# Optimization experiments

Measured on AMD Instinct MI355X. Metric: run time of the kernel, lower is better.

## Reference

```python
import jax, jax.numpy as jnp
import numpy as np

N = 8192
D_IN = 1024
D_OUT = 1024


def setup_inputs() -> dict:
    key = jax.random.key(0)
    ks = jax.random.split(key, 7)
    s = 1.0 / np.sqrt(D_IN)
    return {
        "feat": jax.random.normal(ks[0], (N, D_IN), dtype=jnp.float32),
        "Wq": jax.random.uniform(ks[1], (D_IN, D_OUT), jnp.float32, -s, s),
        "bq": jax.random.uniform(ks[2], (D_OUT,), jnp.float32, -s, s),
        "Wk": jax.random.uniform(ks[3], (D_IN, D_OUT), jnp.float32, -s, s),
        "bk": jax.random.uniform(ks[4], (D_OUT,), jnp.float32, -s, s),
        "Wv": jax.random.uniform(ks[5], (D_IN, D_OUT), jnp.float32, -s, s),
        "bv": jax.random.uniform(ks[6], (D_OUT,), jnp.float32, -s, s),
    }


def reference(feat, Wq, bq, Wk, bk, Wv, bv):
    # eval mode: dropout(p=0.3, training=False) is identity
    q = feat @ Wq + bq          # [N, D_OUT]
    k = feat @ Wk + bk          # [N, D_OUT]
    v = feat @ Wv + bv          # [N, D_OUT]
    scale = 1.0 / jnp.sqrt(jnp.float32(D_OUT))
    scores = (q @ k.T) * scale  # [N, N]
    attn = jax.nn.softmax(scores, axis=1)
    return attn @ v             # [N, D_OUT]
```

## Files before the change

### kernel.cpp

```cpp
#include <hip/hip_runtime.h>
#include <hip/hip_bf16.h>
#include <stdint.h>

typedef __hip_bfloat16 bf16;
typedef __attribute__((ext_vector_type(8))) short short8;
typedef __attribute__((ext_vector_type(4))) float f32x4;

#define BM 128
#define BN 128

__device__ __forceinline__ unsigned short f2bf_bits(float x) {
    return __builtin_bit_cast(unsigned short, __float2bfloat16(x));
}

__device__ __forceinline__ void gload_lds16(const bf16* g, bf16* l) {
    __builtin_amdgcn_global_load_lds(
        (const __attribute__((address_space(1))) void*)(const void*)g,
        (__attribute__((address_space(3))) void*)(void*)l,
        16, 0, 0);
}

__global__ void cvt_f32_bf16_x4(const float* __restrict__ in, unsigned short* __restrict__ out, int n4) {
    int i = blockIdx.x * 256 + threadIdx.x;
    if (i < n4) {
        float4 v = reinterpret_cast<const float4*>(in)[i];
        ushort4 o;
        o.x = f2bf_bits(v.x); o.y = f2bf_bits(v.y);
        o.z = f2bf_bits(v.z); o.w = f2bf_bits(v.w);
        reinterpret_cast<ushort4*>(out)[i] = o;
    }
}

__global__ void wtrans_kernel(const float* __restrict__ W0, const float* __restrict__ W1,
                              const float* __restrict__ W2, bf16* __restrict__ Wt) {
    __shared__ float tile[32][33];
    const int z = blockIdx.z;
    const float* in = (z == 0) ? W0 : (z == 1) ? W1 : W2;
    bf16* out = Wt + (size_t)z * 1024 * 1024;
    const int bx = blockIdx.x, by = blockIdx.y, tx = threadIdx.x;
    for (int r = threadIdx.y; r < 32; r += 8)
        tile[r][tx] = in[(size_t)(by * 32 + r) * 1024 + bx * 32 + tx];
    __syncthreads();
    for (int r = threadIdx.y; r < 32; r += 8)
        out[(size_t)(bx * 32 + r) * 1024 + by * 32 + tx] = __float2bfloat16(tile[tx][r]);
}

__global__ void tpose_bf16(const bf16* __restrict__ in, bf16* __restrict__ out, int rows, int cols) {
    __shared__ bf16 tile[32][33];
    const int bx = blockIdx.x, by = blockIdx.y, tx = threadIdx.x;
    for (int r = threadIdx.y; r < 32; r += 8)
        tile[r][tx] = in[(size_t)(by * 32 + r) * cols + bx * 32 + tx];
    __syncthreads();
    for (int r = threadIdx.y; r < 32; r += 8)
        out[(size_t)(bx * 32 + r) * rows + by * 32 + tx] = tile[tx][r];
}

__global__ void scale_rows(float* __restrict__ out, const float* __restrict__ lsum) {
    int i = blockIdx.x * 256 + threadIdx.x;
    float4 v = reinterpret_cast<float4*>(out)[i];
    float inv = 1.0f / lsum[i >> 8];
    v.x *= inv; v.y *= inv; v.z *= inv; v.w *= inv;
    reinterpret_cast<float4*>(out)[i] = v;
}

template <int MODE, int KH, int SWAP>
__global__ __launch_bounds__(256, 4)
void gemm_bt(const bf16* __restrict__ A, const bf16* __restrict__ B,
             const float* __restrict__ b0, const float* __restrict__ b1,
             const float* __restrict__ b2, float* __restrict__ lsum,
             bf16* __restrict__ outb, float* __restrict__ outf,
             int M, int N, int K, int ldb, int ldout, float scale) {
    constexpr int TILE = 128 * 32;
    constexpr int SELEMS = (2 * KH * TILE < 9216) ? 9216 : 2 * KH * TILE;
    __shared__ bf16 smem[SELEMS];
    bf16* As = smem;
    bf16* Bs = smem + KH * TILE;

    const int tid  = threadIdx.x;
    const int lane = tid & 63;
    const int wave = tid >> 6;
    const int wm = wave & 1, wn = wave >> 1;
    const int l16  = lane & 15;
    const int quad = lane >> 4;
    long bm0, bn0;
    if (SWAP == 2) {
        const int lin = blockIdx.y * 8 + blockIdx.x;
        const int xcd = lin & 7;
        const int s   = lin >> 3;
        bn0 = (long)(s & 7) * BN;
        bm0 = (long)((s >> 3) * 8 + xcd) * BM;
    } else {
        bm0 = (long)(SWAP ? blockIdx.y : blockIdx.x) * BM;
        bn0 = (long)(SWAP ? blockIdx.x : blockIdx.y) * BN;
    }

    const float* bias = nullptr;
    if (MODE == 0) {
        const int z = blockIdx.z;
        B    += (size_t)z * N * K;
        outb += (size_t)z * M * ldout;
        bias  = (z == 0) ? b0 : (z == 1) ? b1 : b2;
    }

    const int lrow = lane >> 2;
    const int lcol = (lane & 3) * 8;
    const bf16* gA[2][KH];
    const bf16* gB[2][KH];
    bf16* lA[2][KH];
    bf16* lB[2][KH];
#pragma unroll
    for (int u = 0; u < 2; u++)
#pragma unroll
        for (int h = 0; h < KH; h++) {
            gA[u][h] = A + (size_t)(bm0 + wave * 32 + u * 16 + lrow) * K + h * 32 + lcol;
            gB[u][h] = B + (size_t)(bn0 + wave * 32 + u * 16 + lrow) * ldb + h * 32 + lcol;
            lA[u][h] = As + h * TILE + (wave * 32 + u * 16) * 32;
            lB[u][h] = Bs + h * TILE + (wave * 32 + u * 16) * 32;
        }

    const bf16* Ard = As + (wm * 64 + l16) * 32 + quad * 8;
    const bf16* Brd = Bs + (wn * 64 + l16) * 32 + quad * 8;

    f32x4 acc[4][4];
    const f32x4 zero = {0.f, 0.f, 0.f, 0.f};
#pragma unroll
    for (int i = 0; i < 4; i++)
#pragma unroll
        for (int j = 0; j < 4; j++) acc[i][j] = zero;

    for (int k0 = 0; k0 < K; k0 += KH * 32) {
        __syncthreads();
#pragma unroll
        for (int u = 0; u < 2; u++)
#pragma unroll
            for (int h = 0; h < KH; h++) {
                gload_lds16(gA[u][h] + k0, lA[u][h]);
                gload_lds16(gB[u][h] + k0, lB[u][h]);
            }
        __syncthreads();
#pragma unroll
        for (int h = 0; h < KH; h++) {
            short8 af[4], bfr[4];
#pragma unroll
            for (int mi = 0; mi < 4; mi++)
                af[mi] = *reinterpret_cast<const short8*>(Ard + h * TILE + mi * 16 * 32);
#pragma unroll
            for (int ni = 0; ni < 4; ni++)
                bfr[ni] = *reinterpret_cast<const short8*>(Brd + h * TILE + ni * 16 * 32);
#pragma unroll
            for (int mi = 0; mi < 4; mi++)
#pragma unroll
                for (int ni = 0; ni < 4; ni++)
                    acc[mi][ni] = __builtin_amdgcn_mfma_f32_16x16x32_bf16(af[mi], bfr[ni], acc[mi][ni], 0, 0, 0);
        }
    }

    if (MODE == 0 || MODE == 1) {
        __syncthreads();
        bf16* eb = smem + wave * 1152;
        float bcol[4];
        if (MODE == 0) {
#pragma unroll
            for (int ni = 0; ni < 4; ni++) bcol[ni] = bias[bn0 + wn * 64 + l16 + ni * 16];
        }
#pragma unroll
        for (int mi = 0; mi < 4; mi++) {
#pragma unroll
            for (int r = 0; r < 4; r++) {
                float s = 0.f;
#pragma unroll
                for (int ni = 0; ni < 4; ni++) {
                    float v = acc[mi][ni][r];
                    if (MODE == 0) v += bcol[ni];
                    else { v = __expf(v * scale); s += v; }
                    eb[(quad * 4 + r) * 72 + ni * 16 + l16] = __float2bfloat16(v);
                }
                if (MODE == 1) {
                    s += __shfl_xor(s, 1);
                    s += __shfl_xor(s, 2);
                    s += __shfl_xor(s, 4);
                    s += __shfl_xor(s, 8);
                    if (l16 == 0) atomicAdd(&lsum[bm0 + wm * 64 + mi * 16 + quad * 4 + r], s);
                }
            }
            asm volatile("s_waitcnt lgkmcnt(0)" ::: "memory");
#pragma unroll
            for (int p = 0; p < 2; p++) {
                int r2 = p * 8 + (lane >> 3);
                int c2 = (lane & 7) * 8;
                short8 val = *reinterpret_cast<const short8*>(eb + r2 * 72 + c2);
                *reinterpret_cast<short8*>(
                    outb + (size_t)(bm0 + wm * 64 + mi * 16 + r2) * ldout + bn0 + wn * 64 + c2) = val;
            }
            asm volatile("s_waitcnt lgkmcnt(0)" ::: "memory");
        }
    } else {
        const int rb2 = wm * 64 + quad * 4;
        const int cb2 = wn * 64 + l16;
#pragma unroll
        for (int mi = 0; mi < 4; mi++)
#pragma unroll
            for (int r = 0; r < 4; r++) {
                long row = bm0 + rb2 + mi * 16 + r;
                float mul = (MODE == 3) ? 1.0f / lsum[row] : 0.f;
#pragma unroll
                for (int ni = 0; ni < 4; ni++) {
                    long col = bn0 + cb2 + ni * 16;
                    if (MODE == 3) outf[row * ldout + col] = acc[mi][ni][r] * mul;
                    else           outf[row * ldout + col] += acc[mi][ni][r];
                }
            }
    }
}

extern "C" void kernel_launch(void* const* d_in, const int* in_sizes, int n_in,
                              void* d_out, int out_size, void* d_ws, size_t ws_size,
                              hipStream_t stream) {
    const float* feat = (const float*)d_in[0];
    const float* Wq   = (const float*)d_in[1];
    const float* bqv  = (const float*)d_in[2];
    const float* Wk   = (const float*)d_in[3];
    const float* bkv  = (const float*)d_in[4];
    const float* Wv   = (const float*)d_in[5];
    const float* bvv  = (const float*)d_in[6];
    float* outp = (float*)d_out;

    const int M = 8192, D = 1024;
    char* ws = (char*)d_ws;
    size_t off = 0;
    auto carve = [&](size_t bytes) -> char* {
        char* r = ws + off;
        off += (bytes + 255) & ~(size_t)255;
        return r;
    };
    bf16* featb = (bf16*)carve((size_t)M * D * 2);
    bf16* Wbt   = (bf16*)carve((size_t)3 * D * D * 2);
    bf16* qkv   = (bf16*)carve((size_t)3 * M * D * 2);
    float* lsum = (float*)carve((size_t)M * 4);
    bf16* vbt   = featb;
    size_t avail = (ws_size > off) ? ws_size - off : 0;

    int C;
    if      (avail >= (size_t)M * M * 2)    C = M;
    else if (avail >= (size_t)M * 4096 * 2) C = 4096;
    else if (avail >= (size_t)M * 2048 * 2) C = 2048;
    else                                    C = 1024;
    bf16* Pc = (bf16*)carve((size_t)M * C * 2);

    {
        int n4 = M * D / 4;
        cvt_f32_bf16_x4<<<dim3((n4 + 255) / 256), dim3(256), 0, stream>>>(feat, (unsigned short*)featb, n4);
    }
    wtrans_kernel<<<dim3(32, 32, 3), dim3(32, 8), 0, stream>>>(Wq, Wk, Wv, Wbt);
    gemm_bt<0, 2, 0><<<dim3(M / 128, D / 128, 3), dim3(256), 0, stream>>>(
        featb, Wbt, bqv, bkv, bvv, nullptr, qkv, nullptr, M, D, D, D, D, 1.0f);
    tpose_bf16<<<dim3(D / 32, M / 32), dim3(32, 8), 0, stream>>>(qkv + (size_t)2 * M * D, vbt, M, D);
    hipMemsetAsync(lsum, 0, (size_t)M * 4, stream);

    const float scale = 0.03125f;
    bf16* qb = qkv;
    bf16* kb = qkv + (size_t)M * D;
    if (C == M) {
        gemm_bt<1, 2, 0><<<dim3(M / 128, M / 128), dim3(256), 0, stream>>>(
            qb, kb, nullptr, nullptr, nullptr, lsum, Pc, nullptr, M, M, D, D, M, scale);
        gemm_bt<3, 2, 2><<<dim3(D / 128, M / 128), dim3(256), 0, stream>>>(
            Pc, vbt, nullptr, nullptr, nullptr, lsum, nullptr, outp, M, D, M, M, D, 0.f);
    } else {
        hipMemsetAsync(outp, 0, (size_t)M * D * 4, stream);
        for (int c = 0; c < M / C; c++) {
            gemm_bt<1, 2, 0><<<dim3(M / 128, C / 128), dim3(256), 0, stream>>>(
                qb, kb + (size_t)c * C * D, nullptr, nullptr, nullptr, lsum, Pc, nullptr,
                M, C, D, D, C, scale);
            gemm_bt<2, 2, 1><<<dim3(D / 128, M / 128), dim3(256), 0, stream>>>(
                Pc, vbt + (size_t)c * C, nullptr, nullptr, nullptr, nullptr, nullptr, outp,
                M, D, C, M, D, 0.f);
        }
        scale_rows<<<dim3(M * D / 4 / 256), dim3(256), 0, stream>>>(outp, lsum);
    }
}
```

Measured before the change: 449.5 us.

## Split-K the PV GEMM with atomic accumulation and fuse prep kernels

Merges the feature conversion, weight transpose and lsum zeroing into a single prep launch to cut launch overhead. The attn@V GEMM (512 blocks, K=8192) is split into two K halves along grid z, so twice as many blocks run. The halves are accumulated into a zeroed output with float atomicAdd, and normalisation moves to a separate scale_rows pass. The trade-off is an extra memset, atomic traffic on an 8192x1024 fp32 output, and an extra read/write pass over the output.

```diff
diff --git a/kernel.cpp b/kernel.cpp
--- a/kernel.cpp
+++ b/kernel.cpp
@@ -20,29 +20,36 @@
         16, 0, 0);
 }
 
-__global__ void cvt_f32_bf16_x4(const float* __restrict__ in, unsigned short* __restrict__ out, int n4) {
-    int i = blockIdx.x * 256 + threadIdx.x;
-    if (i < n4) {
-        float4 v = reinterpret_cast<const float4*>(in)[i];
+__global__ void prep_kernel(const float* __restrict__ feat, unsigned short* __restrict__ featb,
+                            const float* __restrict__ W0, const float* __restrict__ W1,
+                            const float* __restrict__ W2, bf16* __restrict__ Wt,
+                            float* __restrict__ lsum) {
+    const int b = blockIdx.x;
+    const int tid = threadIdx.x;
+    if (b < 8192) {
+        int i = b * 256 + tid;
+        float4 v = reinterpret_cast<const float4*>(feat)[i];
         ushort4 o;
         o.x = f2bf_bits(v.x); o.y = f2bf_bits(v.y);
         o.z = f2bf_bits(v.z); o.w = f2bf_bits(v.w);
-        reinterpret_cast<ushort4*>(out)[i] = o;
-    }
-}
-
-__global__ void wtrans_kernel(const float* __restrict__ W0, const float* __restrict__ W1,
-                              const float* __restrict__ W2, bf16* __restrict__ Wt) {
-    __shared__ float tile[32][33];
-    const int z = blockIdx.z;
-    const float* in = (z == 0) ? W0 : (z == 1) ? W1 : W2;
-    bf16* out = Wt + (size_t)z * 1024 * 1024;
-    const int bx = blockIdx.x, by = blockIdx.y, tx = threadIdx.x;
-    for (int r = threadIdx.y; r < 32; r += 8)
-        tile[r][tx] = in[(size_t)(by * 32 + r) * 1024 + bx * 32 + tx];
-    __syncthreads();
-    for (int r = threadIdx.y; r < 32; r += 8)
-        out[(size_t)(bx * 32 + r) * 1024 + by * 32 + tx] = __float2bfloat16(tile[tx][r]);
+        reinterpret_cast<ushort4*>(featb)[i] = o;
+    } else if (b < 11264) {
+        __shared__ float tile[32][33];
+        const int b2 = b - 8192;
+        const int z = b2 >> 10;
+        const int t = b2 & 1023;
+        const int bx = t & 31, by = t >> 5;
+        const int tx = tid & 31, ty = tid >> 5;
+        const float* in = (z == 0) ? W0 : (z == 1) ? W1 : W2;
+        bf16* out = Wt + (size_t)z * 1024 * 1024;
+        for (int r = ty; r < 32; r += 8)
+            tile[r][tx] = in[(size_t)(by * 32 + r) * 1024 + bx * 32 + tx];
+        __syncthreads();
+        for (int r = ty; r < 32; r += 8)
+            out[(size_t)(bx * 32 + r) * 1024 + by * 32 + tx] = __float2bfloat16(tile[tx][r]);
+    } else {
+        for (int i = tid; i < 8192; i += 256) lsum[i] = 0.f;
+    }
 }
 
 __global__ void tpose_bf16(const bf16* __restrict__ in, bf16* __restrict__ out, int rows, int cols) {
@@ -102,6 +109,9 @@
         bias  = (z == 0) ? b0 : (z == 1) ? b1 : b2;
     }
 
+    const int  ksp   = (MODE == 4) ? (K >> 1) : K;
+    const long k0beg = (MODE == 4) ? (long)blockIdx.z * ksp : 0;
+
     const int lrow = lane >> 2;
     const int lcol = (lane & 3) * 8;
     const bf16* gA[2][KH];
@@ -128,7 +138,7 @@
 #pragma unroll
         for (int j = 0; j < 4; j++) acc[i][j] = zero;
 
-    for (int k0 = 0; k0 < K; k0 += KH * 32) {
+    for (long k0 = k0beg; k0 < k0beg + ksp; k0 += KH * 32) {
         __syncthreads();
 #pragma unroll
         for (int u = 0; u < 2; u++)
@@ -206,8 +216,9 @@
 #pragma unroll
                 for (int ni = 0; ni < 4; ni++) {
                     long col = bn0 + cb2 + ni * 16;
-                    if (MODE == 3) outf[row * ldout + col] = acc[mi][ni][r] * mul;
-                    else           outf[row * ldout + col] += acc[mi][ni][r];
+                    if (MODE == 3)      outf[row * ldout + col] = acc[mi][ni][r] * mul;
+                    else if (MODE == 4) atomicAdd(&outf[row * ldout + col], acc[mi][ni][r]);
+                    else                outf[row * ldout + col] += acc[mi][ni][r];
                 }
             }
     }
@@ -247,15 +258,11 @@
     else                                    C = 1024;
     bf16* Pc = (bf16*)carve((size_t)M * C * 2);
 
-    {
-        int n4 = M * D / 4;
-        cvt_f32_bf16_x4<<<dim3((n4 + 255) / 256), dim3(256), 0, stream>>>(feat, (unsigned short*)featb, n4);
-    }
-    wtrans_kernel<<<dim3(32, 32, 3), dim3(32, 8), 0, stream>>>(Wq, Wk, Wv, Wbt);
+    prep_kernel<<<dim3(11265), dim3(256), 0, stream>>>(
+        feat, (unsigned short*)featb, Wq, Wk, Wv, Wbt, lsum);
     gemm_bt<0, 2, 0><<<dim3(M / 128, D / 128, 3), dim3(256), 0, stream>>>(
         featb, Wbt, bqv, bkv, bvv, nullptr, qkv, nullptr, M, D, D, D, D, 1.0f);
     tpose_bf16<<<dim3(D / 32, M / 32), dim3(32, 8), 0, stream>>>(qkv + (size_t)2 * M * D, vbt, M, D);
-    hipMemsetAsync(lsum, 0, (size_t)M * 4, stream);
 
     const float scale = 0.03125f;
     bf16* qb = qkv;
@@ -263,8 +270,10 @@
     if (C == M) {
         gemm_bt<1, 2, 0><<<dim3(M / 128, M / 128), dim3(256), 0, stream>>>(
             qb, kb, nullptr, nullptr, nullptr, lsum, Pc, nullptr, M, M, D, D, M, scale);
-        gemm_bt<3, 2, 2><<<dim3(D / 128, M / 128), dim3(256), 0, stream>>>(
-            Pc, vbt, nullptr, nullptr, nullptr, lsum, nullptr, outp, M, D, M, M, D, 0.f);
+        hipMemsetAsync(outp, 0, (size_t)M * D * 4, stream);
+        gemm_bt<4, 2, 2><<<dim3(D / 128, M / 128, 2), dim3(256), 0, stream>>>(
+            Pc, vbt, nullptr, nullptr, nullptr, nullptr, nullptr, outp, M, D, M, M, D, 0.f);
+        scale_rows<<<dim3(M * D / 4 / 256), dim3(256), 0, stream>>>(outp, lsum);
     } else {
         hipMemsetAsync(outp, 0, (size_t)M * D * 4, stream);
         for (int c = 0; c < M / C; c++) {
```

New measurement: 476.1 us. +5.9%, slower.
